# Kernel optimization log

Measured on AMD Instinct MI355X. Metric: run time of the kernel, lower is better.

Reference implementation:

```python
import jax, jax.numpy as jnp
import numpy as np

NP_, NA, NPR = 3000, 25, 1071
N = NP_ + NA + NPR          # 4096 total nodes
D = 256                     # latent_dim
H = 8                       # num_heads
DH = D // H                 # head dim 32
FF = 4 * D                  # feed-forward dim
BLOCKS = 3                  # args.block_num
E = 131072                  # edges = N * 32 avg degree
EPS = 1e-5


def setup_inputs() -> dict:
    key = jax.random.key(0)
    ks = jax.random.split(key, 16)
    s = 1.0 / np.sqrt(D)
    return {
        "adj_row": jax.random.randint(ks[0], (E,), 0, N, dtype=jnp.int32),
        "adj_col": jax.random.randint(ks[1], (E,), 0, N, dtype=jnp.int32),
        "adj_val": jax.random.uniform(ks[2], (E,), dtype=jnp.float32),
        "pe": jax.random.normal(ks[3], (NP_, D), dtype=jnp.float32) * s,
        "ae": jax.random.normal(ks[4], (NA, D), dtype=jnp.float32) * s,
        "qe": jax.random.normal(ks[5], (NPR, D), dtype=jnp.float32) * s,
        "Wqkv": jax.random.normal(ks[6], (D, 3 * D), dtype=jnp.float32) * s,
        "Wo": jax.random.normal(ks[7], (D, D), dtype=jnp.float32) * s,
        "W1": jax.random.normal(ks[8], (D, FF), dtype=jnp.float32) * s,
        "b1": jnp.zeros((FF,), dtype=jnp.float32),
        "W2": jax.random.normal(ks[9], (FF, D), dtype=jnp.float32) * (1.0 / np.sqrt(FF)),
        "b2": jnp.zeros((D,), dtype=jnp.float32),
        "ln1_g": jnp.ones((D,), dtype=jnp.float32),
        "ln1_b": jnp.zeros((D,), dtype=jnp.float32),
        "ln2_g": jnp.ones((D,), dtype=jnp.float32),
        "ln2_b": jnp.zeros((D,), dtype=jnp.float32),
    }


def _layer_norm(x, g, b):
    m = jnp.mean(x, axis=-1, keepdims=True)
    v = jnp.mean(jnp.square(x - m), axis=-1, keepdims=True)
    return (x - m) * jax.lax.rsqrt(v + EPS) * g + b


def _encoder_layer(x, Wqkv, Wo, W1, b1, W2, b2, ln1_g, ln1_b, ln2_g, ln2_b):
    # x: [N, D]; standard post-LN transformer encoder (dropout = 0)
    qkv = x @ Wqkv                                   # [N, 3D]
    q, k, v = jnp.split(qkv, 3, axis=-1)
    q = q.reshape(N, H, DH)
    k = k.reshape(N, H, DH)
    v = v.reshape(N, H, DH)
    scores = jnp.einsum("nhd,mhd->hnm", q, k) / np.sqrt(DH)  # [H, N, N]
    att = jax.nn.softmax(scores, axis=-1)
    o = jnp.einsum("hnm,mhd->nhd", att, v).reshape(N, D) @ Wo
    x = _layer_norm(x + o, ln1_g, ln1_b)
    h = jax.nn.relu(x @ W1 + b1) @ W2 + b2
    return _layer_norm(x + h, ln2_g, ln2_b)


def _spmm(adj_row, adj_col, adj_val, x):
    # sparse [N,N] @ dense [N,D] via gather + segment-sum scatter
    msgs = adj_val[:, None] * x[adj_col]             # [E, D]
    return jax.ops.segment_sum(msgs, adj_row, num_segments=N)


def reference(adj_row, adj_col, adj_val, pe, ae, qe, Wqkv, Wo, W1, b1, W2, b2,
              ln1_g, ln1_b, ln2_g, ln2_b):
    cur = jnp.concatenate([pe, ae, qe], axis=0)      # [N, D]
    total = cur
    for _ in range(BLOCKS):
        t = _spmm(adj_row, adj_col, adj_val, cur)
        t = _encoder_layer(t, Wqkv, Wo, W1, b1, W2, b2, ln1_g, ln1_b, ln2_g, ln2_b)
        cur = t + cur                                # residual per block
        total = total + cur                          # sum over embeds list
    protein = total[:NP_]
    aa = total[NP_:NP_ + NA]
    prop = total[NP_ + NA:]
    return total, protein, aa, prop
```

## Files before the change

kernel.cpp:

```cpp
#include <hip/hip_runtime.h>
#include <hip/hip_bf16.h>


#define NPROT 3000
#define NAA   25
#define NPROP 1071
#define NTOT  4096
#define DIM   256
#define NH    8
#define DHD   32
#define FFD   1024
#define NEDGE 131072
#define LNEPS 1e-5f
#define KSPLIT 2
#define KVQ (NTOT/KSPLIT)

typedef unsigned short u16;
typedef unsigned int u32;
typedef __attribute__((ext_vector_type(8))) short short8v;
typedef __attribute__((ext_vector_type(4))) float float4v;
typedef __attribute__((ext_vector_type(2))) unsigned int uint2v;

__device__ __forceinline__ u16 f2bu(float x){
  union { __hip_bfloat16 h; u16 u; } c; c.h = __float2bfloat16(x); return c.u;
}
__device__ __forceinline__ float bu2f(u16 u){
  union { u32 i; float f; } c; c.i = ((u32)u) << 16; return c.f;
}
__device__ __forceinline__ float4v mfma16(short8v a, short8v b, float4v c){
  return __builtin_amdgcn_mfma_f32_16x16x32_bf16(a, b, c, 0, 0, 0);
}
__device__ __forceinline__ u32 packbf(float lo, float hi){
  u32 ul = __builtin_bit_cast(u32, lo);
  u32 uh = __builtin_bit_cast(u32, hi);
  return (ul >> 16) | (uh & 0xFFFF0000u);
}
__device__ __forceinline__ void gload_lds16(const u16* g, u16* l){
  __builtin_amdgcn_global_load_lds(
      (const __attribute__((address_space(1))) void*)g,
      (__attribute__((address_space(3))) void*)l, 16, 0, 0);
}

__global__ __launch_bounds__(256) void k_embed(const float* __restrict__ pe, const float* __restrict__ ae,
                                               const float* __restrict__ qe,
                                               float* __restrict__ cur, float* __restrict__ tot,
                                               u16* __restrict__ curb){
  int i = blockIdx.x*256 + threadIdx.x;
  int row = i >> 8;
  float v;
  if (row < NPROT)           v = pe[i];
  else if (row < NPROT+NAA)  v = ae[i - NPROT*DIM];
  else                       v = qe[i - (NPROT+NAA)*DIM];
  cur[i] = v; tot[i] = v; curb[i] = f2bu(v);
}

__global__ __launch_bounds__(256) void k_zero(int* __restrict__ p, int n){
  int i = blockIdx.x*256 + threadIdx.x; if (i < n) p[i] = 0;
}

__global__ __launch_bounds__(256) void k_wconv_all(const float* __restrict__ Wqkv, const float* __restrict__ Wo,
                                                   const float* __restrict__ W1, const float* __restrict__ W2,
                                                   u16* __restrict__ wqkvt, u16* __restrict__ wot,
                                                   u16* __restrict__ w1t, u16* __restrict__ w2t){
  int b = blockIdx.x;
  const float* W; u16* Wt; int K, N, n;
  if (b < 768)       { W = Wqkv; Wt = wqkvt; K = 256;  N = 768;  n = b; }
  else if (b < 1024) { W = Wo;   Wt = wot;   K = 256;  N = 256;  n = b - 768; }
  else if (b < 2048) { W = W1;   Wt = w1t;   K = 256;  N = 1024; n = b - 1024; }
  else               { W = W2;   Wt = w2t;   K = 1024; N = 256;  n = b - 2048; }
  for (int k = threadIdx.x; k < K; k += 256)
    Wt[(size_t)n*K + k] = f2bu(W[(size_t)k*N + n]);
}

__global__ __launch_bounds__(256) void k_hist(const int* __restrict__ rows, int* __restrict__ cnt){
  int e = blockIdx.x*256 + threadIdx.x; if (e < NEDGE) atomicAdd(&cnt[rows[e]], 1);
}

__global__ __launch_bounds__(64) void k_scan(const int* __restrict__ cnt, int* __restrict__ rowptr,
                                             int* __restrict__ cursor){
  int lane = threadIdx.x;
  int sum = 0;
  for (int i = 0; i < 64; ++i) sum += cnt[lane*64 + i];
  int pref = sum;
  #pragma unroll
  for (int off = 1; off < 64; off <<= 1){
    int u = __shfl_up(pref, off);
    if (lane >= off) pref += u;
  }
  int run = pref - sum;
  for (int i = 0; i < 64; ++i){
    int c = cnt[lane*64 + i];
    rowptr[lane*64 + i] = run;
    cursor[lane*64 + i] = run;
    run += c;
  }
  if (lane == 63) rowptr[NTOT] = run;
}

__global__ __launch_bounds__(256) void k_scatter(const int* __restrict__ rows, const int* __restrict__ cols,
                                                 const float* __restrict__ vals, int* __restrict__ cursor,
                                                 int* __restrict__ ccol, float* __restrict__ cval){
  int e = blockIdx.x*256 + threadIdx.x; if (e >= NEDGE) return;
  int p = atomicAdd(&cursor[rows[e]], 1);
  ccol[p] = cols[e]; cval[p] = vals[e];
}

__global__ __launch_bounds__(256) void k_spmm(const int* __restrict__ rowptr, const int* __restrict__ ccol,
                                              const float* __restrict__ cval, const u16* __restrict__ xb,
                                              float* __restrict__ out, u16* __restrict__ outb){
  int r = blockIdx.x, c = threadIdx.x;
  int s = rowptr[r], e = rowptr[r+1];
  float acc = 0.f;
  for (int i = s; i < e; ++i)
    acc += cval[i] * bu2f(xb[((size_t)ccol[i] << 8) + c]);
  out[((size_t)r << 8) + c] = acc;
  outb[((size_t)r << 8) + c] = f2bu(acc);
}

template<int RELU, int BIAS, int BF16OUT, int MERGE>
__global__ __launch_bounds__(256) void k_gemm64(const u16* __restrict__ A, const u16* __restrict__ Wt,
                                                const float* __restrict__ bias, void* __restrict__ Cv,
                                                const float* __restrict__ mbuf, const float* __restrict__ lbuf,
                                                int M, int K, int Nc){
  __shared__ u16 Al[64*64];
  __shared__ u16 Bl[64*64];
  const int tid = threadIdx.x;
  const int w  = tid >> 6, l = tid & 63, lr = l & 15, g = l >> 4;
  const int row0 = blockIdx.y*64, col0 = blockIdx.x*64;
  const int wm = (w >> 1)*32, wn = (w & 1)*32;
  const int sm = tid >> 2;
  const int so = (tid & 3)*2;
  const int srow = (l >> 3);
  const int soct = (l & 7) ^ srow;
  float4v acc[2][2] = {};

  for (int k0 = 0; k0 < K; k0 += 64){
    if (MERGE){
      const u16* Bs = Wt + (size_t)(col0 + sm)*K + k0 + so*8;
      int row = row0 + sm;
      #pragma unroll
      for (int j = 0; j < 2; ++j){
        int o = so + j;
        int kabs = k0 + o*8;
        int h = kabs >> 5;
        float mm0 = mbuf[(size_t)h*NTOT + row];
        float mm1 = mbuf[(size_t)(NH + h)*NTOT + row];
        float Mx = fmaxf(mm0, mm1);
        float e0 = __expf(mm0 - Mx), e1 = __expf(mm1 - Mx);
        float L = e0*lbuf[(size_t)h*NTOT + row] + e1*lbuf[(size_t)(NH + h)*NTOT + row];
        float sc0 = e0 / L, sc1 = e1 / L;
        short8v p0 = *(const short8v*)(A + (size_t)row*DIM + kabs);
        short8v p1 = *(const short8v*)(A + (size_t)NTOT*DIM + (size_t)row*DIM + kabs);
        short8v mv;
        #pragma unroll
        for (int jj = 0; jj < 8; ++jj)
          mv[jj] = (short)f2bu(sc0*bu2f((u16)p0[jj]) + sc1*bu2f((u16)p1[jj]));
        int slot = o ^ (sm & 7);
        *(short8v*)(Al + sm*64 + slot*8) = mv;
        *(short8v*)(Bl + sm*64 + slot*8) = *(const short8v*)(Bs + j*8);
      }
    } else {
      #pragma unroll
      for (int i = 0; i < 2; ++i){
        int row = 16*w + 8*i + srow;
        gload_lds16(A  + (size_t)(row0 + row)*K + k0 + soct*8, Al + (16*w + 8*i)*64);
        gload_lds16(Wt + (size_t)(col0 + row)*K + k0 + soct*8, Bl + (16*w + 8*i)*64);
      }
    }
    __syncthreads();
    #pragma unroll
    for (int kk = 0; kk < 2; ++kk){
      short8v af[2], bfr[2];
      #pragma unroll
      for (int i = 0; i < 2; ++i){
        int am = wm + 16*i + lr;
        af[i]  = *(const short8v*)(Al + am*64 + (((4*kk + g) ^ (am & 7))*8));
        int bn = wn + 16*i + lr;
        bfr[i] = *(const short8v*)(Bl + bn*64 + (((4*kk + g) ^ (bn & 7))*8));
      }
      acc[0][0] = mfma16(af[0], bfr[0], acc[0][0]);
      acc[0][1] = mfma16(af[0], bfr[1], acc[0][1]);
      acc[1][0] = mfma16(af[1], bfr[0], acc[1][0]);
      acc[1][1] = mfma16(af[1], bfr[1], acc[1][1]);
    }
    __syncthreads();
  }

  #pragma unroll
  for (int mi = 0; mi < 2; ++mi){
    #pragma unroll
    for (int ni = 0; ni < 2; ++ni){
      int col = col0 + wn + 16*ni + lr;
      float bv = BIAS ? bias[col] : 0.f;
      #pragma unroll
      for (int j = 0; j < 4; ++j){
        int row = row0 + wm + 16*mi + 4*g + j;
        float v = acc[mi][ni][j] + bv;
        if (RELU) v = fmaxf(v, 0.f);
        if (BF16OUT) ((u16*)Cv)[(size_t)row*Nc + col] = f2bu(v);
        else         ((float*)Cv)[(size_t)row*Nc + col] = v;
      }
    }
  }
}

__global__ __launch_bounds__(256) void k_attn_mfma(const u16* __restrict__ qbf,
                                                   u16* __restrict__ op,
                                                   float* __restrict__ mbuf, float* __restrict__ lbuf){
  __shared__ u16 Vt[2][32*64];
  __shared__ u16 Pl[4][16*64];
  __shared__ float Fl[4][16];
  const int h   = blockIdx.y;
  const int ks  = blockIdx.z;
  const int qb  = blockIdx.x * 64;
  const int tid = threadIdx.x;
  const int w   = tid >> 6;
  const int l   = tid & 63;
  const int lr  = l & 15;
  const int g   = l >> 4;
  const int sr  = tid >> 2;
  const int sq  = tid & 3;
  const float SC  = 0.17677669529663687f;
  const float SCL = 0.25503837f;
  const float DEFER = 31.368f;
  u16* opart = op + (size_t)ks*NTOT*DIM;

  short8v qf = *(const short8v*)(qbf + (size_t)(qb + 16*w + lr)*768 + h*DHD + 8*g);
  short8v ones;
  #pragma unroll
  for (int j = 0; j < 8; ++j) ones[j] = (short)0x3F80;

  float4v oa0 = {0.f,0.f,0.f,0.f}, oa1 = {0.f,0.f,0.f,0.f};
  float4v accl = {0.f,0.f,0.f,0.f};
  float mrun = -1e30f;
  u16* pw = &Pl[w][0];

  const u16* vp = qbf + (size_t)(ks*KVQ + sr)*768 + 512 + h*DHD + 8*sq;
  const u16* kp = qbf + (size_t)(ks*KVQ + lr)*768 + 256 + h*DHD + 8*g;
  short8v vreg = *(const short8v*)vp;
  short8v kf0 = *(const short8v*)(kp);
  short8v kf1 = *(const short8v*)(kp + (size_t)16*768);
  short8v kf2 = *(const short8v*)(kp + (size_t)32*768);
  short8v kf3 = *(const short8v*)(kp + (size_t)48*768);

  const int NIT = KVQ/64;
  for (int t = 0; t < NIT; ++t){
    u16* vt = &Vt[t & 1][0];
    #pragma unroll
    for (int j = 0; j < 8; ++j){
      int row  = 8*sq + j;
      int slot = (sr >> 3) ^ j;
      vt[row*64 + slot*8 + (sr & 7)] = (u16)vreg[j];
    }
    __syncthreads();
    vp += (size_t)64*768;
    vreg = *(const short8v*)vp;

    float4v s0 = mfma16(kf0, qf, (float4v){0.f,0.f,0.f,0.f});
    float4v s1 = mfma16(kf1, qf, (float4v){0.f,0.f,0.f,0.f});
    float4v s2 = mfma16(kf2, qf, (float4v){0.f,0.f,0.f,0.f});
    float4v s3 = mfma16(kf3, qf, (float4v){0.f,0.f,0.f,0.f});
    kp += (size_t)64*768;
    kf0 = *(const short8v*)(kp);
    kf1 = *(const short8v*)(kp + (size_t)16*768);
    kf2 = *(const short8v*)(kp + (size_t)32*768);
    kf3 = *(const short8v*)(kp + (size_t)48*768);

    float m0 = fmaxf(fmaxf(fmaxf(s0[0],s0[1]),s0[2]),s0[3]);
    float m1 = fmaxf(fmaxf(fmaxf(s1[0],s1[1]),s1[2]),s1[3]);
    float m2 = fmaxf(fmaxf(fmaxf(s2[0],s2[1]),s2[2]),s2[3]);
    float m3 = fmaxf(fmaxf(fmaxf(s3[0],s3[1]),s3[2]),s3[3]);
    float tm = fmaxf(fmaxf(fmaxf(m0,m1),m2),m3);
    tm = fmaxf(tm, __shfl_xor(tm, 16));
    tm = fmaxf(tm, __shfl_xor(tm, 32));
    const bool nomax = __all(tm <= mrun + DEFER);
    float fac = 1.f;
    if (!nomax){
      float mn = fmaxf(mrun, tm);
      fac = exp2f((mrun - mn)*SCL);
      mrun = mn;
    }
    float mns = mrun*SCL;
    #pragma unroll
    for (int j = 0; j < 4; ++j){
      s0[j] = exp2f(__builtin_fmaf(s0[j], SCL, -mns));
      s1[j] = exp2f(__builtin_fmaf(s1[j], SCL, -mns));
      s2[j] = exp2f(__builtin_fmaf(s2[j], SCL, -mns));
      s3[j] = exp2f(__builtin_fmaf(s3[j], SCL, -mns));
    }

    {
      int gh = g >> 1, gl = 4*(g & 1);
      uint2v* d0 = (uint2v*)(pw + lr*64 + ((0 + gh) ^ (lr & 7))*8 + gl);
      uint2v* d1 = (uint2v*)(pw + lr*64 + ((2 + gh) ^ (lr & 7))*8 + gl);
      uint2v* d2 = (uint2v*)(pw + lr*64 + ((4 + gh) ^ (lr & 7))*8 + gl);
      uint2v* d3 = (uint2v*)(pw + lr*64 + ((6 + gh) ^ (lr & 7))*8 + gl);
      *d0 = (uint2v){packbf(s0[0],s0[1]), packbf(s0[2],s0[3])};
      *d1 = (uint2v){packbf(s1[0],s1[1]), packbf(s1[2],s1[3])};
      *d2 = (uint2v){packbf(s2[0],s2[1]), packbf(s2[2],s2[3])};
      *d3 = (uint2v){packbf(s3[0],s3[1]), packbf(s3[2],s3[3])};
    }

    if (!nomax){
      if (g == 0) Fl[w][lr] = fac;
      float fq0 = Fl[w][4*g+0], fq1 = Fl[w][4*g+1], fq2 = Fl[w][4*g+2], fq3 = Fl[w][4*g+3];
      oa0[0]*=fq0; oa0[1]*=fq1; oa0[2]*=fq2; oa0[3]*=fq3;
      oa1[0]*=fq0; oa1[1]*=fq1; oa1[2]*=fq2; oa1[3]*=fq3;
      accl[0]*=fq0; accl[1]*=fq1; accl[2]*=fq2; accl[3]*=fq3;
    }

    #pragma unroll
    for (int kk = 0; kk < 2; ++kk){
      int slotp = (4*kk + g) ^ (lr & 7);
      short8v pa = *(const short8v*)(pw + lr*64 + slotp*8);
      short8v v0 = *(const short8v*)(vt + lr*64        + slotp*8);
      short8v v1 = *(const short8v*)(vt + (lr+16)*64   + slotp*8);
      oa0  = mfma16(pa, v0, oa0);
      oa1  = mfma16(pa, v1, oa1);
      accl = mfma16(pa, ones, accl);
    }
  }

  #pragma unroll
  for (int j = 0; j < 4; ++j){
    size_t row = (size_t)(qb + 16*w + 4*g + j);
    opart[row*DIM + h*DHD + lr]      = f2bu(oa0[j]);
    opart[row*DIM + h*DHD + 16 + lr] = f2bu(oa1[j]);
  }
  if (l < 16){
    size_t mi = (size_t)(ks*NH + h)*NTOT + qb + 16*w + lr;
    mbuf[mi] = mrun*SC;
  }
  if (lr == 0){
    #pragma unroll
    for (int j = 0; j < 4; ++j){
      size_t mi = (size_t)(ks*NH + h)*NTOT + qb + 16*w + 4*g + j;
      lbuf[mi] = accl[j];
    }
  }
}

template<int DUAL>
__global__ __launch_bounds__(256) void k_add_ln(const float* __restrict__ a, const float* __restrict__ b,
                                                const float* __restrict__ g, const float* __restrict__ be,
                                                float* __restrict__ out, u16* __restrict__ out2){
  __shared__ float red[4];
  int r = blockIdx.x, c = threadIdx.x;
  float v = a[((size_t)r << 8) + c] + b[((size_t)r << 8) + c];
  float s = v;
  #pragma unroll
  for (int off = 32; off; off >>= 1) s += __shfl_down(s, off);
  if ((c & 63) == 0) red[c >> 6] = s;
  __syncthreads();
  float mean = (red[0]+red[1]+red[2]+red[3]) * (1.f/DIM);
  __syncthreads();
  float d = v - mean;
  float s2 = d*d;
  #pragma unroll
  for (int off = 32; off; off >>= 1) s2 += __shfl_down(s2, off);
  if ((c & 63) == 0) red[c >> 6] = s2;
  __syncthreads();
  float var = (red[0]+red[1]+red[2]+red[3]) * (1.f/DIM);
  float rv = d * rsqrtf(var + LNEPS) * g[c] + be[c];
  out[((size_t)r << 8) + c] = rv;
  if (DUAL) out2[((size_t)r << 8) + c] = f2bu(rv);
}

template<int FINAL>
__global__ __launch_bounds__(256) void k_add_ln_upd(const float* __restrict__ a, const float* __restrict__ b,
                                                    const float* __restrict__ g, const float* __restrict__ be,
                                                    float* __restrict__ cur, float* __restrict__ tot,
                                                    u16* __restrict__ curb, float* __restrict__ out){
  __shared__ float red[4];
  int r = blockIdx.x, c = threadIdx.x;
  size_t idx = ((size_t)r << 8) + c;
  float v = a[idx] + b[idx];
  float s = v;
  #pragma unroll
  for (int off = 32; off; off >>= 1) s += __shfl_down(s, off);
  if ((c & 63) == 0) red[c >> 6] = s;
  __syncthreads();
  float mean = (red[0]+red[1]+red[2]+red[3]) * (1.f/DIM);
  __syncthreads();
  float d = v - mean;
  float s2 = d*d;
  #pragma unroll
  for (int off = 32; off; off >>= 1) s2 += __shfl_down(s2, off);
  if ((c & 63) == 0) red[c >> 6] = s2;
  __syncthreads();
  float var = (red[0]+red[1]+red[2]+red[3]) * (1.f/DIM);
  float rv = d * rsqrtf(var + LNEPS) * g[c] + be[c];
  float cu = cur[idx] + rv;
  cur[idx] = cu;
  if (!FINAL) curb[idx] = f2bu(cu);
  float tv = tot[idx] + cu;
  tot[idx] = tv;
  if (FINAL){
    out[idx] = tv;
    out[(size_t)NTOT*DIM + idx] = tv;
  }
}

extern "C" void kernel_launch(void* const* d_in, const int* in_sizes, int n_in,
                              void* d_out, int out_size, void* d_ws, size_t ws_size,
                              hipStream_t stream){
  const int*   adj_row = (const int*)  d_in[0];
  const int*   adj_col = (const int*)  d_in[1];
  const float* adj_val = (const float*)d_in[2];
  const float* pe   = (const float*)d_in[3];
  const float* ae   = (const float*)d_in[4];
  const float* qe   = (const float*)d_in[5];
  const float* Wqkv = (const float*)d_in[6];
  const float* Wo   = (const float*)d_in[7];
  const float* W1   = (const float*)d_in[8];
  const float* b1   = (const float*)d_in[9];
  const float* W2   = (const float*)d_in[10];
  const float* b2   = (const float*)d_in[11];
  const float* g1   = (const float*)d_in[12];
  const float* be1  = (const float*)d_in[13];
  const float* g2   = (const float*)d_in[14];
  const float* be2  = (const float*)d_in[15];
  float* out = (float*)d_out;

  char* w = (char*)d_ws;
  float* cur  = (float*)w; w += (size_t)NTOT*DIM*4;
  float* tot  = (float*)w; w += (size_t)NTOT*DIM*4;
  float* tf   = (float*)w; w += (size_t)NTOT*DIM*4;
  float* pbuf = (float*)w; w += (size_t)NTOT*DIM*4;
  float* x1   = (float*)w; w += (size_t)NTOT*DIM*4;
  u16* tbf    = (u16*)w;   w += (size_t)NTOT*DIM*2;
  u16* curb   = (u16*)w;   w += (size_t)NTOT*DIM*2;
  u16* x1b    = (u16*)w;   w += (size_t)NTOT*DIM*2;
  u16* hq     = (u16*)w;   w += (size_t)NTOT*FFD*2;
  u16* wqkvt  = (u16*)w;   w += (size_t)768*256*2;
  u16* wot    = (u16*)w;   w += (size_t)256*256*2;
  u16* w1t    = (u16*)w;   w += (size_t)1024*256*2;
  u16* w2t    = (u16*)w;   w += (size_t)256*1024*2;
  int* rowptr = (int*)w;   w += (size_t)(NTOT+1)*4;
  int* cnt    = (int*)w;   w += (size_t)NTOT*4;
  int* cursor = (int*)w;   w += (size_t)NTOT*4;
  int* ccol   = (int*)w;   w += (size_t)NEDGE*4;
  float* cval = (float*)w; w += (size_t)NEDGE*4;
  u16* qbf  = hq;
  u16* opbf = (u16*)pbuf;
  float* mbuf = (float*)tbf;
  float* lbuf = mbuf + (size_t)KSPLIT*NH*NTOT;

  k_zero<<<16, 256, 0, stream>>>(cnt, NTOT);
  k_embed<<<NTOT, 256, 0, stream>>>(pe, ae, qe, cur, tot, curb);
  k_hist<<<NEDGE/256, 256, 0, stream>>>(adj_row, cnt);
  k_scan<<<1, 64, 0, stream>>>(cnt, rowptr, cursor);
  k_scatter<<<NEDGE/256, 256, 0, stream>>>(adj_row, adj_col, adj_val, cursor, ccol, cval);
  k_wconv_all<<<2304, 256, 0, stream>>>(Wqkv, Wo, W1, W2, wqkvt, wot, w1t, w2t);

  for (int blk = 0; blk < 3; ++blk){
    k_spmm<<<NTOT, 256, 0, stream>>>(rowptr, ccol, cval, curb, tf, tbf);
    k_gemm64<0,0,1,0><<<dim3(768/64, NTOT/64), 256, 0, stream>>>(tbf, wqkvt, nullptr, qbf, nullptr, nullptr, NTOT, 256, 768);
    k_attn_mfma<<<dim3(NTOT/64, NH, KSPLIT), 256, 0, stream>>>(qbf, opbf, mbuf, lbuf);
    k_gemm64<0,0,0,1><<<dim3(256/64, NTOT/64), 256, 0, stream>>>(opbf, wot, nullptr, pbuf, mbuf, lbuf, NTOT, 256, 256);
    k_add_ln<1><<<NTOT, 256, 0, stream>>>(tf, pbuf, g1, be1, x1, x1b);
    k_gemm64<1,1,1,0><<<dim3(1024/64, NTOT/64), 256, 0, stream>>>(x1b, w1t, b1, hq, nullptr, nullptr, NTOT, 256, 1024);
    k_gemm64<0,1,0,0><<<dim3(256/64, NTOT/64), 256, 0, stream>>>(hq, w2t, b2, pbuf, nullptr, nullptr, NTOT, 1024, 256);
    if (blk < 2)
      k_add_ln_upd<0><<<NTOT, 256, 0, stream>>>(x1, pbuf, g2, be2, cur, tot, curb, nullptr);
    else
      k_add_ln_upd<1><<<NTOT, 256, 0, stream>>>(x1, pbuf, g2, be2, cur, tot, nullptr, out);
  }
}
```

Baseline: 469.3 us.

## Process two query tiles per attention block and split keys four ways

Each attention block now handles 128 queries as two 64-row subtiles that share the same K fragments and V tile from shared memory, so every K/V load is reused twice. The key range is split four ways instead of two, which keeps the total block count unchanged. The four partial outputs go into scratch space borrowed from x1, x1b and curb, and the Wo GEMM's merge step now combines four partials with their max/sum statistics. The cost is more registers per thread and more partial-output traffic in the merge.

Result: slower. 481.1 us (+2.5%).

```diff
diff --git a/kernel.cpp b/kernel.cpp
--- a/kernel.cpp
+++ b/kernel.cpp
@@ -12,7 +12,7 @@
 #define FFD   1024
 #define NEDGE 131072
 #define LNEPS 1e-5f
-#define KSPLIT 2
+#define KSPLIT 4
 #define KVQ (NTOT/KSPLIT)
 
 typedef unsigned short u16;
@@ -120,6 +120,8 @@
 template<int RELU, int BIAS, int BF16OUT, int MERGE>
 __global__ __launch_bounds__(256) void k_gemm64(const u16* __restrict__ A, const u16* __restrict__ Wt,
                                                 const float* __restrict__ bias, void* __restrict__ Cv,
+                                                const u16* __restrict__ P0, const u16* __restrict__ P1,
+                                                const u16* __restrict__ P2, const u16* __restrict__ P3,
                                                 const float* __restrict__ mbuf, const float* __restrict__ lbuf,
                                                 int M, int K, int Nc){
   __shared__ u16 Al[64*64];
@@ -142,19 +144,27 @@
       for (int j = 0; j < 2; ++j){
         int o = so + j;
         int kabs = k0 + o*8;
-        int h = kabs >> 5;
-        float mm0 = mbuf[(size_t)h*NTOT + row];
-        float mm1 = mbuf[(size_t)(NH + h)*NTOT + row];
-        float Mx = fmaxf(mm0, mm1);
+        int hh = kabs >> 5;
+        float mm0 = mbuf[(size_t)(0*NH + hh)*NTOT + row];
+        float mm1 = mbuf[(size_t)(1*NH + hh)*NTOT + row];
+        float mm2 = mbuf[(size_t)(2*NH + hh)*NTOT + row];
+        float mm3 = mbuf[(size_t)(3*NH + hh)*NTOT + row];
+        float Mx = fmaxf(fmaxf(mm0, mm1), fmaxf(mm2, mm3));
         float e0 = __expf(mm0 - Mx), e1 = __expf(mm1 - Mx);
-        float L = e0*lbuf[(size_t)h*NTOT + row] + e1*lbuf[(size_t)(NH + h)*NTOT + row];
-        float sc0 = e0 / L, sc1 = e1 / L;
-        short8v p0 = *(const short8v*)(A + (size_t)row*DIM + kabs);
-        short8v p1 = *(const short8v*)(A + (size_t)NTOT*DIM + (size_t)row*DIM + kabs);
+        float e2 = __expf(mm2 - Mx), e3 = __expf(mm3 - Mx);
+        float L = e0*lbuf[(size_t)(0*NH + hh)*NTOT + row] + e1*lbuf[(size_t)(1*NH + hh)*NTOT + row]
+                + e2*lbuf[(size_t)(2*NH + hh)*NTOT + row] + e3*lbuf[(size_t)(3*NH + hh)*NTOT + row];
+        float sc0 = e0 / L, sc1 = e1 / L, sc2 = e2 / L, sc3 = e3 / L;
+        size_t off = (size_t)row*DIM + kabs;
+        short8v q0 = *(const short8v*)(P0 + off);
+        short8v q1 = *(const short8v*)(P1 + off);
+        short8v q2 = *(const short8v*)(P2 + off);
+        short8v q3 = *(const short8v*)(P3 + off);
         short8v mv;
         #pragma unroll
         for (int jj = 0; jj < 8; ++jj)
-          mv[jj] = (short)f2bu(sc0*bu2f((u16)p0[jj]) + sc1*bu2f((u16)p1[jj]));
+          mv[jj] = (short)f2bu(sc0*bu2f((u16)q0[jj]) + sc1*bu2f((u16)q1[jj])
+                             + sc2*bu2f((u16)q2[jj]) + sc3*bu2f((u16)q3[jj]));
         int slot = o ^ (sm & 7);
         *(short8v*)(Al + sm*64 + slot*8) = mv;
         *(short8v*)(Bl + sm*64 + slot*8) = *(const short8v*)(Bs + j*8);
@@ -205,14 +215,15 @@
 }
 
 __global__ __launch_bounds__(256) void k_attn_mfma(const u16* __restrict__ qbf,
-                                                   u16* __restrict__ op,
+                                                   u16* __restrict__ p0, u16* __restrict__ p1,
+                                                   u16* __restrict__ p2, u16* __restrict__ p3,
                                                    float* __restrict__ mbuf, float* __restrict__ lbuf){
   __shared__ u16 Vt[2][32*64];
   __shared__ u16 Pl[4][16*64];
   __shared__ float Fl[4][16];
   const int h   = blockIdx.y;
   const int ks  = blockIdx.z;
-  const int qb  = blockIdx.x * 64;
+  const int qb  = blockIdx.x * 128;
   const int tid = threadIdx.x;
   const int w   = tid >> 6;
   const int l   = tid & 63;
@@ -223,16 +234,17 @@
   const float SC  = 0.17677669529663687f;
   const float SCL = 0.25503837f;
   const float DEFER = 31.368f;
-  u16* opart = op + (size_t)ks*NTOT*DIM;
-
-  short8v qf = *(const short8v*)(qbf + (size_t)(qb + 16*w + lr)*768 + h*DHD + 8*g);
+  u16* opart = (ks == 0) ? p0 : (ks == 1) ? p1 : (ks == 2) ? p2 : p3;
+
+  short8v qfA = *(const short8v*)(qbf + (size_t)(qb + 16*w + lr)*768 + h*DHD + 8*g);
+  short8v qfB = *(const short8v*)(qbf + (size_t)(qb + 64 + 16*w + lr)*768 + h*DHD + 8*g);
   short8v ones;
   #pragma unroll
   for (int j = 0; j < 8; ++j) ones[j] = (short)0x3F80;
 
-  float4v oa0 = {0.f,0.f,0.f,0.f}, oa1 = {0.f,0.f,0.f,0.f};
-  float4v accl = {0.f,0.f,0.f,0.f};
-  float mrun = -1e30f;
+  float4v oaA0 = {0,0,0,0}, oaA1 = {0,0,0,0}, acclA = {0,0,0,0};
+  float4v oaB0 = {0,0,0,0}, oaB1 = {0,0,0,0}, acclB = {0,0,0,0};
+  float mrunA = -1e30f, mrunB = -1e30f;
   u16* pw = &Pl[w][0];
 
   const u16* vp = qbf + (size_t)(ks*KVQ + sr)*768 + 512 + h*DHD + 8*sq;
@@ -242,6 +254,10 @@
   short8v kf1 = *(const short8v*)(kp + (size_t)16*768);
   short8v kf2 = *(const short8v*)(kp + (size_t)32*768);
   short8v kf3 = *(const short8v*)(kp + (size_t)48*768);
+
+  const int gh = g >> 1, gl = 4*(g & 1);
+  const int slotp0 = (0 + g) ^ (lr & 7);
+  const int slotp1 = (4 + g) ^ (lr & 7);
 
   const int NIT = KVQ/64;
   for (int t = 0; t < NIT; ++t){
@@ -256,86 +272,141 @@
     vp += (size_t)64*768;
     vreg = *(const short8v*)vp;
 
-    float4v s0 = mfma16(kf0, qf, (float4v){0.f,0.f,0.f,0.f});
-    float4v s1 = mfma16(kf1, qf, (float4v){0.f,0.f,0.f,0.f});
-    float4v s2 = mfma16(kf2, qf, (float4v){0.f,0.f,0.f,0.f});
-    float4v s3 = mfma16(kf3, qf, (float4v){0.f,0.f,0.f,0.f});
+    float4v sA0 = mfma16(kf0, qfA, (float4v){0,0,0,0});
+    float4v sA1 = mfma16(kf1, qfA, (float4v){0,0,0,0});
+    float4v sA2 = mfma16(kf2, qfA, (float4v){0,0,0,0});
+    float4v sA3 = mfma16(kf3, qfA, (float4v){0,0,0,0});
+    float4v sB0 = mfma16(kf0, qfB, (float4v){0,0,0,0});
+    float4v sB1 = mfma16(kf1, qfB, (float4v){0,0,0,0});
+    float4v sB2 = mfma16(kf2, qfB, (float4v){0,0,0,0});
+    float4v sB3 = mfma16(kf3, qfB, (float4v){0,0,0,0});
     kp += (size_t)64*768;
     kf0 = *(const short8v*)(kp);
     kf1 = *(const short8v*)(kp + (size_t)16*768);
     kf2 = *(const short8v*)(kp + (size_t)32*768);
     kf3 = *(const short8v*)(kp + (size_t)48*768);
 
-    float m0 = fmaxf(fmaxf(fmaxf(s0[0],s0[1]),s0[2]),s0[3]);
-    float m1 = fmaxf(fmaxf(fmaxf(s1[0],s1[1]),s1[2]),s1[3]);
-    float m2 = fmaxf(fmaxf(fmaxf(s2[0],s2[1]),s2[2]),s2[3]);
-    float m3 = fmaxf(fmaxf(fmaxf(s3[0],s3[1]),s3[2]),s3[3]);
-    float tm = fmaxf(fmaxf(fmaxf(m0,m1),m2),m3);
-    tm = fmaxf(tm, __shfl_xor(tm, 16));
-    tm = fmaxf(tm, __shfl_xor(tm, 32));
-    const bool nomax = __all(tm <= mrun + DEFER);
-    float fac = 1.f;
-    if (!nomax){
-      float mn = fmaxf(mrun, tm);
-      fac = exp2f((mrun - mn)*SCL);
-      mrun = mn;
-    }
-    float mns = mrun*SCL;
-    #pragma unroll
-    for (int j = 0; j < 4; ++j){
-      s0[j] = exp2f(__builtin_fmaf(s0[j], SCL, -mns));
-      s1[j] = exp2f(__builtin_fmaf(s1[j], SCL, -mns));
-      s2[j] = exp2f(__builtin_fmaf(s2[j], SCL, -mns));
-      s3[j] = exp2f(__builtin_fmaf(s3[j], SCL, -mns));
-    }
+    short8v v00 = *(const short8v*)(vt + lr*64      + slotp0*8);
+    short8v v10 = *(const short8v*)(vt + (lr+16)*64 + slotp0*8);
+    short8v v01 = *(const short8v*)(vt + lr*64      + slotp1*8);
+    short8v v11 = *(const short8v*)(vt + (lr+16)*64 + slotp1*8);
 
     {
-      int gh = g >> 1, gl = 4*(g & 1);
+      float m0 = fmaxf(fmaxf(fmaxf(sA0[0],sA0[1]),sA0[2]),sA0[3]);
+      float m1 = fmaxf(fmaxf(fmaxf(sA1[0],sA1[1]),sA1[2]),sA1[3]);
+      float m2 = fmaxf(fmaxf(fmaxf(sA2[0],sA2[1]),sA2[2]),sA2[3]);
+      float m3 = fmaxf(fmaxf(fmaxf(sA3[0],sA3[1]),sA3[2]),sA3[3]);
+      float tm = fmaxf(fmaxf(fmaxf(m0,m1),m2),m3);
+      tm = fmaxf(tm, __shfl_xor(tm, 16));
+      tm = fmaxf(tm, __shfl_xor(tm, 32));
+      const bool nomax = __all(tm <= mrunA + DEFER);
+      float fac = 1.f;
+      if (!nomax){
+        float mn = fmaxf(mrunA, tm);
+        fac = exp2f((mrunA - mn)*SCL);
+        mrunA = mn;
+      }
+      float mns = mrunA*SCL;
+      #pragma unroll
+      for (int j = 0; j < 4; ++j){
+        sA0[j] = exp2f(__builtin_fmaf(sA0[j], SCL, -mns));
+        sA1[j] = exp2f(__builtin_fmaf(sA1[j], SCL, -mns));
+        sA2[j] = exp2f(__builtin_fmaf(sA2[j], SCL, -mns));
+        sA3[j] = exp2f(__builtin_fmaf(sA3[j], SCL, -mns));
+      }
       uint2v* d0 = (uint2v*)(pw + lr*64 + ((0 + gh) ^ (lr & 7))*8 + gl);
       uint2v* d1 = (uint2v*)(pw + lr*64 + ((2 + gh) ^ (lr & 7))*8 + gl);
       uint2v* d2 = (uint2v*)(pw + lr*64 + ((4 + gh) ^ (lr & 7))*8 + gl);
       uint2v* d3 = (uint2v*)(pw + lr*64 + ((6 + gh) ^ (lr & 7))*8 + gl);
-      *d0 = (uint2v){packbf(s0[0],s0[1]), packbf(s0[2],s0[3])};
-      *d1 = (uint2v){packbf(s1[0],s1[1]), packbf(s1[2],s1[3])};
-      *d2 = (uint2v){packbf(s2[0],s2[1]), packbf(s2[2],s2[3])};
-      *d3 = (uint2v){packbf(s3[0],s3[1]), packbf(s3[2],s3[3])};
-    }
-
-    if (!nomax){
-      if (g == 0) Fl[w][lr] = fac;
-      float fq0 = Fl[w][4*g+0], fq1 = Fl[w][4*g+1], fq2 = Fl[w][4*g+2], fq3 = Fl[w][4*g+3];
-      oa0[0]*=fq0; oa0[1]*=fq1; oa0[2]*=fq2; oa0[3]*=fq3;
-      oa1[0]*=fq0; oa1[1]*=fq1; oa1[2]*=fq2; oa1[3]*=fq3;
-      accl[0]*=fq0; accl[1]*=fq1; accl[2]*=fq2; accl[3]*=fq3;
-    }
-
-    #pragma unroll
-    for (int kk = 0; kk < 2; ++kk){
-      int slotp = (4*kk + g) ^ (lr & 7);
-      short8v pa = *(const short8v*)(pw + lr*64 + slotp*8);
-      short8v v0 = *(const short8v*)(vt + lr*64        + slotp*8);
-      short8v v1 = *(const short8v*)(vt + (lr+16)*64   + slotp*8);
-      oa0  = mfma16(pa, v0, oa0);
-      oa1  = mfma16(pa, v1, oa1);
-      accl = mfma16(pa, ones, accl);
+      *d0 = (uint2v){packbf(sA0[0],sA0[1]), packbf(sA0[2],sA0[3])};
+      *d1 = (uint2v){packbf(sA1[0],sA1[1]), packbf(sA1[2],sA1[3])};
+      *d2 = (uint2v){packbf(sA2[0],sA2[1]), packbf(sA2[2],sA2[3])};
+      *d3 = (uint2v){packbf(sA3[0],sA3[1]), packbf(sA3[2],sA3[3])};
+      if (!nomax){
+        if (g == 0) Fl[w][lr] = fac;
+        float fq0 = Fl[w][4*g+0], fq1 = Fl[w][4*g+1], fq2 = Fl[w][4*g+2], fq3 = Fl[w][4*g+3];
+        oaA0[0]*=fq0; oaA0[1]*=fq1; oaA0[2]*=fq2; oaA0[3]*=fq3;
+        oaA1[0]*=fq0; oaA1[1]*=fq1; oaA1[2]*=fq2; oaA1[3]*=fq3;
+        acclA[0]*=fq0; acclA[1]*=fq1; acclA[2]*=fq2; acclA[3]*=fq3;
+      }
+      short8v pa0 = *(const short8v*)(pw + lr*64 + slotp0*8);
+      short8v pa1 = *(const short8v*)(pw + lr*64 + slotp1*8);
+      oaA0  = mfma16(pa0, v00, oaA0);
+      oaA1  = mfma16(pa0, v10, oaA1);
+      acclA = mfma16(pa0, ones, acclA);
+      oaA0  = mfma16(pa1, v01, oaA0);
+      oaA1  = mfma16(pa1, v11, oaA1);
+      acclA = mfma16(pa1, ones, acclA);
+    }
+    {
+      float m0 = fmaxf(fmaxf(fmaxf(sB0[0],sB0[1]),sB0[2]),sB0[3]);
+      float m1 = fmaxf(fmaxf(fmaxf(sB1[0],sB1[1]),sB1[2]),sB1[3]);
+      float m2 = fmaxf(fmaxf(fmaxf(sB2[0],sB2[1]),sB2[2]),sB2[3]);
+      float m3 = fmaxf(fmaxf(fmaxf(sB3[0],sB3[1]),sB3[2]),sB3[3]);
+      float tm = fmaxf(fmaxf(fmaxf(m0,m1),m2),m3);
+      tm = fmaxf(tm, __shfl_xor(tm, 16));
+      tm = fmaxf(tm, __shfl_xor(tm, 32));
+      const bool nomax = __all(tm <= mrunB + DEFER);
+      float fac = 1.f;
+      if (!nomax){
+        float mn = fmaxf(mrunB, tm);
+        fac = exp2f((mrunB - mn)*SCL);
+        mrunB = mn;
+      }
+      float mns = mrunB*SCL;
+      #pragma unroll
+      for (int j = 0; j < 4; ++j){
+        sB0[j] = exp2f(__builtin_fmaf(sB0[j], SCL, -mns));
+        sB1[j] = exp2f(__builtin_fmaf(sB1[j], SCL, -mns));
+        sB2[j] = exp2f(__builtin_fmaf(sB2[j], SCL, -mns));
+        sB3[j] = exp2f(__builtin_fmaf(sB3[j], SCL, -mns));
+      }
+      uint2v* d0 = (uint2v*)(pw + lr*64 + ((0 + gh) ^ (lr & 7))*8 + gl);
+      uint2v* d1 = (uint2v*)(pw + lr*64 + ((2 + gh) ^ (lr & 7))*8 + gl);
+      uint2v* d2 = (uint2v*)(pw + lr*64 + ((4 + gh) ^ (lr & 7))*8 + gl);
+      uint2v* d3 = (uint2v*)(pw + lr*64 + ((6 + gh) ^ (lr & 7))*8 + gl);
+      *d0 = (uint2v){packbf(sB0[0],sB0[1]), packbf(sB0[2],sB0[3])};
+      *d1 = (uint2v){packbf(sB1[0],sB1[1]), packbf(sB1[2],sB1[3])};
+      *d2 = (uint2v){packbf(sB2[0],sB2[1]), packbf(sB2[2],sB2[3])};
+      *d3 = (uint2v){packbf(sB3[0],sB3[1]), packbf(sB3[2],sB3[3])};
+      if (!nomax){
+        if (g == 0) Fl[w][lr] = fac;
+        float fq0 = Fl[w][4*g+0], fq1 = Fl[w][4*g+1], fq2 = Fl[w][4*g+2], fq3 = Fl[w][4*g+3];
+        oaB0[0]*=fq0; oaB0[1]*=fq1; oaB0[2]*=fq2; oaB0[3]*=fq3;
+        oaB1[0]*=fq0; oaB1[1]*=fq1; oaB1[2]*=fq2; oaB1[3]*=fq3;
+        acclB[0]*=fq0; acclB[1]*=fq1; acclB[2]*=fq2; acclB[3]*=fq3;
+      }
+      short8v pa0 = *(const short8v*)(pw + lr*64 + slotp0*8);
+      short8v pa1 = *(const short8v*)(pw + lr*64 + slotp1*8);
+      oaB0  = mfma16(pa0, v00, oaB0);
+      oaB1  = mfma16(pa0, v10, oaB1);
+      acclB = mfma16(pa0, ones, acclB);
+      oaB0  = mfma16(pa1, v01, oaB0);
+      oaB1  = mfma16(pa1, v11, oaB1);
+      acclB = mfma16(pa1, ones, acclB);
     }
   }
 
   #pragma unroll
   for (int j = 0; j < 4; ++j){
-    size_t row = (size_t)(qb + 16*w + 4*g + j);
-    opart[row*DIM + h*DHD + lr]      = f2bu(oa0[j]);
-    opart[row*DIM + h*DHD + 16 + lr] = f2bu(oa1[j]);
+    size_t rowA = (size_t)(qb + 16*w + 4*g + j);
+    size_t rowB = rowA + 64;
+    opart[rowA*DIM + h*DHD + lr]      = f2bu(oaA0[j]);
+    opart[rowA*DIM + h*DHD + 16 + lr] = f2bu(oaA1[j]);
+    opart[rowB*DIM + h*DHD + lr]      = f2bu(oaB0[j]);
+    opart[rowB*DIM + h*DHD + 16 + lr] = f2bu(oaB1[j]);
   }
   if (l < 16){
-    size_t mi = (size_t)(ks*NH + h)*NTOT + qb + 16*w + lr;
-    mbuf[mi] = mrun*SC;
+    size_t miA = (size_t)(ks*NH + h)*NTOT + qb + 16*w + lr;
+    mbuf[miA]      = mrunA*SC;
+    mbuf[miA + 64] = mrunB*SC;
   }
   if (lr == 0){
     #pragma unroll
     for (int j = 0; j < 4; ++j){
-      size_t mi = (size_t)(ks*NH + h)*NTOT + qb + 16*w + 4*g + j;
-      lbuf[mi] = accl[j];
+      size_t miA = (size_t)(ks*NH + h)*NTOT + qb + 16*w + 4*g + j;
+      lbuf[miA]      = acclA[j];
+      lbuf[miA + 64] = acclB[j];
     }
   }
 }
@@ -441,8 +512,11 @@
   int* cursor = (int*)w;   w += (size_t)NTOT*4;
   int* ccol   = (int*)w;   w += (size_t)NEDGE*4;
   float* cval = (float*)w; w += (size_t)NEDGE*4;
-  u16* qbf  = hq;
-  u16* opbf = (u16*)pbuf;
+  u16* qbf = hq;
+  u16* pp0 = (u16*)x1;
+  u16* pp1 = (u16*)x1 + (size_t)NTOT*DIM;
+  u16* pp2 = x1b;
+  u16* pp3 = curb;
   float* mbuf = (float*)tbf;
   float* lbuf = mbuf + (size_t)KSPLIT*NH*NTOT;
 
@@ -455,12 +529,16 @@
 
   for (int blk = 0; blk < 3; ++blk){
     k_spmm<<<NTOT, 256, 0, stream>>>(rowptr, ccol, cval, curb, tf, tbf);
-    k_gemm64<0,0,1,0><<<dim3(768/64, NTOT/64), 256, 0, stream>>>(tbf, wqkvt, nullptr, qbf, nullptr, nullptr, NTOT, 256, 768);
-    k_attn_mfma<<<dim3(NTOT/64, NH, KSPLIT), 256, 0, stream>>>(qbf, opbf, mbuf, lbuf);
-    k_gemm64<0,0,0,1><<<dim3(256/64, NTOT/64), 256, 0, stream>>>(opbf, wot, nullptr, pbuf, mbuf, lbuf, NTOT, 256, 256);
+    k_gemm64<0,0,1,0><<<dim3(768/64, NTOT/64), 256, 0, stream>>>(tbf, wqkvt, nullptr, qbf,
+        nullptr, nullptr, nullptr, nullptr, nullptr, nullptr, NTOT, 256, 768);
+    k_attn_mfma<<<dim3(NTOT/128, NH, KSPLIT), 256, 0, stream>>>(qbf, pp0, pp1, pp2, pp3, mbuf, lbuf);
+    k_gemm64<0,0,0,1><<<dim3(256/64, NTOT/64), 256, 0, stream>>>(nullptr, wot, nullptr, pbuf,
+        pp0, pp1, pp2, pp3, mbuf, lbuf, NTOT, 256, 256);
     k_add_ln<1><<<NTOT, 256, 0, stream>>>(tf, pbuf, g1, be1, x1, x1b);
-    k_gemm64<1,1,1,0><<<dim3(1024/64, NTOT/64), 256, 0, stream>>>(x1b, w1t, b1, hq, nullptr, nullptr, NTOT, 256, 1024);
-    k_gemm64<0,1,0,0><<<dim3(256/64, NTOT/64), 256, 0, stream>>>(hq, w2t, b2, pbuf, nullptr, nullptr, NTOT, 1024, 256);
+    k_gemm64<1,1,1,0><<<dim3(1024/64, NTOT/64), 256, 0, stream>>>(x1b, w1t, b1, hq,
+        nullptr, nullptr, nullptr, nullptr, nullptr, nullptr, NTOT, 256, 1024);
+    k_gemm64<0,1,0,0><<<dim3(256/64, NTOT/64), 256, 0, stream>>>(hq, w2t, b2, pbuf,
+        nullptr, nullptr, nullptr, nullptr, nullptr, nullptr, NTOT, 1024, 256);
     if (blk < 2)
       k_add_ln_upd<0><<<NTOT, 256, 0, stream>>>(x1, pbuf, g2, be2, cur, tot, curb, nullptr);
     else
```
